# Kernel tuning notes

Measured on AMD Instinct MI355X. Metric: run time of the kernel, lower is better.

## Reference

```python
import jax, jax.numpy as jnp
import numpy as np


def setup_inputs() -> dict:
    key = jax.random.key(0)
    kx, kd = jax.random.split(key)
    B, S, D = 32, 1024, 512
    x = jax.random.normal(kx, (B, S, D), dtype=jnp.float32)
    # per-token repeat counts in [1, 9): mean ~4.5 frames per phoneme
    durations = jax.random.randint(kd, (B, S), 1, 9, dtype=jnp.int32)
    return {"x": x, "durations": durations}


def reference(x, durations):
    """Duration-based token expansion (FastSpeech LengthRegulator).

    Replaces the per-token repeat/cat/pad Python loops with a single
    vectorized gather driven by cumulative duration offsets.
    Returns (expanded_x, mel_len, mel_mask) matching the torch module's
    (expanded_x, target=None, mel_len, mel_mask) with target omitted
    (projection is None in this configuration).
    """
    B, S, D = x.shape
    csum = jnp.cumsum(durations, axis=1)          # [B,S] end offset of each token
    mel_len = csum[:, -1]                         # [B]
    # max_len is data-dependent, same as the torch module's max over batch.
    max_len = int(jax.device_get(jnp.max(mel_len)))
    t = jnp.arange(max_len)                       # [T]
    # output frame t belongs to token j iff csum[j-1] <= t < csum[j]
    idx = jax.vmap(lambda c: jnp.searchsorted(c, t, side="right"))(csum)  # [B,T]
    idx = jnp.minimum(idx, S - 1)                 # clamp padding region
    expanded = jnp.take_along_axis(x, idx[:, :, None], axis=1)  # [B,T,D]
    mel_mask = t[None, :] >= mel_len[:, None]     # [B,T] True where padded
    expanded = jnp.where(mel_mask[:, :, None], jnp.zeros((), x.dtype), expanded)
    return expanded, mel_len, mel_mask
```

## Files before the change

### kernel.cpp

```cpp
#include <hip/hip_runtime.h>
#include <hip/hip_bf16.h>


#define S_TOK 1024
#define B_SZ  32

typedef float vfloat4 __attribute__((ext_vector_type(4)));

__global__ __launch_bounds__(64)
void lr_scan_kernel(const int* __restrict__ dur,
                    int* __restrict__ csum,
                    float* __restrict__ mel_len_out) {
    const int b = blockIdx.x;
    const int lane = threadIdx.x;
    const int* __restrict__ d = dur + b * S_TOK;

    int v[16];
    int sum = 0;
#pragma unroll
    for (int k = 0; k < 16; ++k) {
        v[k] = d[lane * 16 + k];
        sum += v[k];
    }
    int run = 0;
#pragma unroll
    for (int k = 0; k < 16; ++k) { run += v[k]; v[k] = run; }

    int tot = sum;
#pragma unroll
    for (int off = 1; off < 64; off <<= 1) {
        int n = __shfl_up(tot, off, 64);
        if (lane >= off) tot += n;
    }
    const int excl = tot - sum;

#pragma unroll
    for (int k = 0; k < 16; ++k)
        csum[b * S_TOK + lane * 16 + k] = v[k] + excl;
    if (lane == 63) mel_len_out[b] = (float)tot;
}

__global__ __launch_bounds__(128)
void lr_fused_kernel(const float* __restrict__ x,
                     const int* __restrict__ csum,
                     float* __restrict__ out,
                     float* __restrict__ mask,
                     int D, int max_len) {
    const int b = blockIdx.y;
    const int tid = threadIdx.x;
    const int* __restrict__ c = csum + b * S_TOK;
    const int d4 = D >> 2;

    if (blockIdx.x < S_TOK) {
        const int s = blockIdx.x;
        const int base = (s == 0) ? 0 : c[s - 1];
        const int dur = c[s] - base;

        const vfloat4 v =
            ((const vfloat4*)(x + ((size_t)b * S_TOK + s) * (size_t)D))[tid];
        vfloat4* __restrict__ o =
            (vfloat4*)(out + ((size_t)b * max_len + base) * (size_t)D) + tid;
        for (int r = 0; r < dur; ++r)
            __builtin_nontemporal_store(v, o + (size_t)r * d4);
        if (tid < dur)
            mask[(size_t)b * max_len + base + tid] = 0.0f;
    } else {
        const int mel = c[S_TOK - 1];
        const int t0 = mel + (blockIdx.x - S_TOK) * 4;
        if (t0 >= max_len) return;
        const vfloat4 z = (vfloat4)(0.f);
#pragma unroll
        for (int k = 0; k < 4; ++k) {
            const int t = t0 + k;
            if (t < max_len) {
                vfloat4* __restrict__ o =
                    (vfloat4*)(out + ((size_t)b * max_len + t) * (size_t)D) + tid;
                __builtin_nontemporal_store(z, o);
            }
        }
        if (tid < 4 && t0 + tid < max_len)
            mask[(size_t)b * max_len + t0 + tid] = 1.0f;
    }
}

extern "C" void kernel_launch(void* const* d_in, const int* in_sizes, int n_in,
                              void* d_out, int out_size, void* d_ws, size_t ws_size,
                              hipStream_t stream) {
    const float* x = (const float*)d_in[0];
    const int* dur = (const int*)d_in[1];
    float* out = (float*)d_out;

    const int D = in_sizes[0] / in_sizes[1];
    const int max_len = (out_size / B_SZ - 1) / (D + 1);

    int* csum = (int*)d_ws;
    float* mel_len = out + (size_t)B_SZ * max_len * D;
    float* mask = mel_len + B_SZ;

    lr_scan_kernel<<<B_SZ, 64, 0, stream>>>(dur, csum, mel_len);

    const int tail_blocks = (max_len > S_TOK) ? ((max_len - S_TOK + 3) / 4 + 1) : 1;
    dim3 fgrid((unsigned)(S_TOK + tail_blocks), (unsigned)B_SZ);
    lr_fused_kernel<<<fgrid, 128, 0, stream>>>(x, csum, out, mask, D, max_len);
}
```

Measured before the change: 353.1 us.

## Parallelize expansion over output frames instead of input tokens

Replaces the per-token block grid (one 128-thread block per source token plus tail blocks) with a fixed 64x32 grid of 256-thread blocks. Each block stages the batch's cumulative sums in shared memory and splits its contiguous range of output frames between two halves. Each half binary-searches its starting token, then walks forward, reloading the source row only when the token changes. This is meant to balance the write work evenly and cut the launch and scheduling cost of about 33k tiny blocks, but it leaves only 2048 blocks with long serial loops, which may underfill the memory pipeline.

```diff
diff --git a/kernel.cpp b/kernel.cpp
--- a/kernel.cpp
+++ b/kernel.cpp
@@ -4,6 +4,7 @@
 
 #define S_TOK 1024
 #define B_SZ  32
+#define NBX   64
 
 typedef float vfloat4 __attribute__((ext_vector_type(4)));
 
@@ -40,47 +41,59 @@
     if (lane == 63) mel_len_out[b] = (float)tot;
 }
 
-__global__ __launch_bounds__(128)
-void lr_fused_kernel(const float* __restrict__ x,
+__global__ __launch_bounds__(256)
+void lr_write_kernel(const float* __restrict__ x,
                      const int* __restrict__ csum,
                      float* __restrict__ out,
                      float* __restrict__ mask,
                      int D, int max_len) {
     const int b = blockIdx.y;
     const int tid = threadIdx.x;
-    const int* __restrict__ c = csum + b * S_TOK;
-    const int d4 = D >> 2;
+    const int half = tid >> 7;
+    const int lane = tid & 127;
 
-    if (blockIdx.x < S_TOK) {
-        const int s = blockIdx.x;
-        const int base = (s == 0) ? 0 : c[s - 1];
-        const int dur = c[s] - base;
+    __shared__ __align__(16) int cs[S_TOK];
+    ((int4*)cs)[tid] = ((const int4*)(csum + b * S_TOK))[tid];
+    __syncthreads();
+    const int mel = cs[S_TOK - 1];
 
-        const vfloat4 v =
-            ((const vfloat4*)(x + ((size_t)b * S_TOK + s) * (size_t)D))[tid];
-        vfloat4* __restrict__ o =
-            (vfloat4*)(out + ((size_t)b * max_len + base) * (size_t)D) + tid;
-        for (int r = 0; r < dur; ++r)
-            __builtin_nontemporal_store(v, o + (size_t)r * d4);
-        if (tid < dur)
-            mask[(size_t)b * max_len + base + tid] = 0.0f;
-    } else {
-        const int mel = c[S_TOK - 1];
-        const int t0 = mel + (blockIdx.x - S_TOK) * 4;
-        if (t0 >= max_len) return;
-        const vfloat4 z = (vfloat4)(0.f);
-#pragma unroll
-        for (int k = 0; k < 4; ++k) {
-            const int t = t0 + k;
-            if (t < max_len) {
-                vfloat4* __restrict__ o =
-                    (vfloat4*)(out + ((size_t)b * max_len + t) * (size_t)D) + tid;
-                __builtin_nontemporal_store(z, o);
+    const int F = (max_len + NBX - 1) / NBX;
+    const int t0 = blockIdx.x * F;
+    const int tEnd = min(t0 + F, max_len);
+    const int hF = (F + 1) >> 1;
+    int t = min(t0 + half * hF, max_len);
+    const int tend = min(t0 + (half ? F : hF), max_len);
+
+    const float* __restrict__ xb = x + (size_t)b * S_TOK * (size_t)D;
+    float* __restrict__ ob = out + (size_t)b * max_len * (size_t)D;
+
+    const int dataEnd = min(tend, mel);
+
+    if (t < dataEnd) {
+        int lo = 0, hi = S_TOK;
+        while (lo < hi) {
+            int mid = (lo + hi) >> 1;
+            if (cs[mid] > t) hi = mid; else lo = mid + 1;
+        }
+        int s = lo;
+        vfloat4 v = ((const vfloat4*)(xb + (size_t)s * D))[lane];
+        int cur = s;
+        for (; t < dataEnd; ++t) {
+            while (cs[s] <= t) ++s;
+            if (s != cur) {
+                v = ((const vfloat4*)(xb + (size_t)s * D))[lane];
+                cur = s;
             }
+            __builtin_nontemporal_store(v, (vfloat4*)(ob + (size_t)t * D) + lane);
         }
-        if (tid < 4 && t0 + tid < max_len)
-            mask[(size_t)b * max_len + t0 + tid] = 1.0f;
     }
+    const vfloat4 z = (vfloat4)(0.f);
+    for (; t < tend; ++t)
+        __builtin_nontemporal_store(z, (vfloat4*)(ob + (size_t)t * D) + lane);
+
+    float* __restrict__ mb = mask + (size_t)b * max_len;
+    for (int u = t0 + tid; u < tEnd; u += 256)
+        mb[u] = (u >= mel) ? 1.0f : 0.0f;
 }
 
 extern "C" void kernel_launch(void* const* d_in, const int* in_sizes, int n_in,
@@ -99,7 +112,6 @@
 
     lr_scan_kernel<<<B_SZ, 64, 0, stream>>>(dur, csum, mel_len);
 
-    const int tail_blocks = (max_len > S_TOK) ? ((max_len - S_TOK + 3) / 4 + 1) : 1;
-    dim3 fgrid((unsigned)(S_TOK + tail_blocks), (unsigned)B_SZ);
-    lr_fused_kernel<<<fgrid, 128, 0, stream>>>(x, csum, out, mask, D, max_len);
+    dim3 grid(NBX, B_SZ);
+    lr_write_kernel<<<grid, 256, 0, stream>>>(x, csum, out, mask, D, max_len);
 }
```

Result: slower. 363.1 us (+2.8%).
